# Kernel optimization log

Measured on AMD Instinct MI355X. Metric: run time of the kernel, lower is better.

The kernel has to match this reference:

```python
import jax, jax.numpy as jnp
import numpy as np
from jax import lax

H = 20  # hidden_size


def _rnn_layer(x_seq, h0, W_ih, W_hh, b_ih, b_hh):
    """Vanilla tanh RNN layer. x_seq: [B,T,D], h0: [B,H]. Returns ([B,T,H], [B,H])."""
    # Precompute input projection for all timesteps (the only large GEMM).
    xp = jnp.einsum('btd,hd->bth', x_seq, W_ih) + b_ih + b_hh  # [B,T,H]

    def step(h, xt):
        h = jnp.tanh(xt + h @ W_hh.T)
        return h, h

    h_last, hs = lax.scan(step, h0, jnp.swapaxes(xp, 0, 1))  # hs: [T,B,H]
    return jnp.swapaxes(hs, 0, 1), h_last


def setup_inputs() -> dict:
    key = jax.random.key(0)
    ks = jax.random.split(key, 12)
    B, T = 4096, 512
    s = 1.0 / np.sqrt(H)  # PyTorch default uniform(-1/sqrt(H), 1/sqrt(H))
    u = lambda k, shape: jax.random.uniform(k, shape, jnp.float32, -s, s)
    return {
        'x': jax.random.normal(ks[0], (B, T, 1), jnp.float32),
        'hidden': jax.random.normal(ks[1], (2, B, H), jnp.float32),
        'W_ih0': u(ks[2], (H, 1)),
        'W_hh0': u(ks[3], (H, H)),
        'b_ih0': u(ks[4], (H,)),
        'b_hh0': u(ks[5], (H,)),
        'W_ih1': u(ks[6], (H, H)),
        'W_hh1': u(ks[7], (H, H)),
        'b_ih1': u(ks[8], (H,)),
        'b_hh1': u(ks[9], (H,)),
        'fc_w': u(ks[10], (1, H)),
        'fc_b': u(ks[11], (1,)),
    }


def reference(x, hidden, W_ih0, W_hh0, b_ih0, b_hh0, W_ih1, W_hh1, b_ih1, b_hh1, fc_w, fc_b):
    # 2-layer vanilla RNN (eval mode: inter-layer dropout disabled)
    h0_seq, h0_last = _rnn_layer(x, hidden[0], W_ih0, W_hh0, b_ih0, b_hh0)
    h1_seq, h1_last = _rnn_layer(h0_seq, hidden[1], W_ih1, W_hh1, b_ih1, b_hh1)
    out = h1_seq[:, -1, :] @ fc_w.T + fc_b  # [B,1]
    new_hidden = jnp.stack([h0_last, h1_last], axis=0)  # [2,B,H]
    return out, new_hidden
```

## Files before the change

### kernel.cpp

```cpp
#include <hip/hip_runtime.h>


#define Bsz 4096
#define Tn  512
#define Hn  20
#define GB  3
#define XPAD 520
#define NTHREADS 64

typedef float v2 __attribute__((ext_vector_type(2)));

__device__ __forceinline__ float tanh_fast(float v) {
    float e = __expf(2.0f * v);
    return 1.0f - 2.0f * __builtin_amdgcn_rcpf(e + 1.0f);
}

#define DOT20P(acc, accb, W, H) do { \
    acc  = __builtin_elementwise_fma(W##0, H##0, acc);  \
    accb = __builtin_elementwise_fma(W##1, H##1, accb); \
    acc  = __builtin_elementwise_fma(W##2, H##2, acc);  \
    accb = __builtin_elementwise_fma(W##3, H##3, accb); \
    acc  = __builtin_elementwise_fma(W##4, H##4, acc);  \
    accb = __builtin_elementwise_fma(W##5, H##5, accb); \
    acc  = __builtin_elementwise_fma(W##6, H##6, acc);  \
    accb = __builtin_elementwise_fma(W##7, H##7, accb); \
    acc  = __builtin_elementwise_fma(W##8, H##8, acc);  \
    accb = __builtin_elementwise_fma(W##9, H##9, accb); \
} while (0)

#define LOAD_ROWP(W, ptr) \
    v2 W##0, W##1, W##2, W##3, W##4, W##5, W##6, W##7, W##8, W##9; \
    { const float4* _p = (const float4*)(ptr); \
      float4 _t; \
      _t = _p[0]; W##0 = (v2){_t.x, _t.y}; W##1 = (v2){_t.z, _t.w}; \
      _t = _p[1]; W##2 = (v2){_t.x, _t.y}; W##3 = (v2){_t.z, _t.w}; \
      _t = _p[2]; W##4 = (v2){_t.x, _t.y}; W##5 = (v2){_t.z, _t.w}; \
      _t = _p[3]; W##6 = (v2){_t.x, _t.y}; W##7 = (v2){_t.z, _t.w}; \
      _t = _p[4]; W##8 = (v2){_t.x, _t.y}; W##9 = (v2){_t.z, _t.w}; }

#define READ_H(H, base) \
    v2 H##0, H##1, H##2, H##3, H##4, H##5, H##6, H##7, H##8, H##9; \
    { const float4 _a = *(const float4*)((base) + 0);  \
      const float4 _b = *(const float4*)((base) + 4);  \
      const float4 _c = *(const float4*)((base) + 8);  \
      const float4 _d = *(const float4*)((base) + 12); \
      const float4 _e = *(const float4*)((base) + 16); \
      H##0 = (v2){_a.x, _a.y}; H##1 = (v2){_a.z, _a.w}; \
      H##2 = (v2){_b.x, _b.y}; H##3 = (v2){_b.z, _b.w}; \
      H##4 = (v2){_c.x, _c.y}; H##5 = (v2){_c.z, _c.w}; \
      H##6 = (v2){_d.x, _d.y}; H##7 = (v2){_d.z, _d.w}; \
      H##8 = (v2){_e.x, _e.y}; H##9 = (v2){_e.z, _e.w}; }

__global__ __launch_bounds__(NTHREADS)
__attribute__((amdgpu_waves_per_eu(1, 2)))
void rnn2_fused(const float* __restrict__ x,
                const float* __restrict__ hidden,
                const float* __restrict__ W_ih0,
                const float* __restrict__ W_hh0,
                const float* __restrict__ b_ih0,
                const float* __restrict__ b_hh0,
                const float* __restrict__ W_ih1,
                const float* __restrict__ W_hh1,
                const float* __restrict__ b_ih1,
                const float* __restrict__ b_hh1,
                const float* __restrict__ fc_w,
                const float* __restrict__ fc_b,
                float* __restrict__ out)
{
    const int tid = threadIdx.x;
    int g = tid / Hn;
    int j = tid - g * Hn;
    const bool lane_ok = (tid < GB * Hn);
    if (!lane_ok) g = GB - 1;
    const int  b        = blockIdx.x * GB + g;
    const bool b_ok     = (b < Bsz);
    const int  bl       = b_ok ? b : (Bsz - 1);
    const bool store_ok = lane_ok && b_ok;

    __shared__ float xs[GB][XPAD];
    __shared__ float hs[2][GB][Hn];

    LOAD_ROWP(w0, W_hh0 + j * Hn)
    LOAD_ROWP(w1, W_ih1 + j * Hn)
    LOAD_ROWP(w2, W_hh1 + j * Hn)

    const float wih0  = W_ih0[j];
    const float bias0 = b_ih0[j] + b_hh0[j];
    const float bias1 = b_ih1[j] + b_hh1[j];

    {
        const int bB = blockIdx.x * GB;
        #pragma unroll
        for (int r = 0; r < (GB * Tn) / (NTHREADS * 4); ++r) {
            const int c  = (r * NTHREADS + tid) * 4;
            const int gg = c >> 9;
            const int t  = c & (Tn - 1);
            const int bb = (bB + gg < Bsz) ? (bB + gg) : (Bsz - 1);
            float4 v = *(const float4*)(x + (long)bb * Tn + t);
            *(float4*)&xs[gg][t] = v;
        }
    }

    hs[0][g][j] = hidden[bl * Hn + j];
    hs[1][g][j] = hidden[(long)Bsz * Hn + bl * Hn + j];

    {
        READ_H(hA, &hs[0][g][0])
        v2 a0  = (v2){fmaf(xs[g][0], wih0, bias0), 0.f};
        v2 a0b = (v2){0.f, 0.f};
        DOT20P(a0, a0b, w0, hA);
        v2 s0 = a0 + a0b;
        hs[0][g][j] = tanh_fast(s0.x + s0.y);
    }

    #pragma unroll 1
    for (int i = 1; i < Tn; ++i) {
        READ_H(hA, &hs[0][g][0])
        READ_H(hB, &hs[1][g][0])

        const float xt = xs[g][i];

        v2 a0  = (v2){fmaf(xt, wih0, bias0), 0.f};
        v2 a0b = (v2){0.f, 0.f};
        v2 a1  = (v2){bias1, 0.f};
        v2 a1b = (v2){0.f, 0.f};
        v2 a2  = (v2){0.f, 0.f};
        v2 a2b = (v2){0.f, 0.f};
        DOT20P(a0, a0b, w0, hA);
        DOT20P(a1, a1b, w1, hA);
        DOT20P(a2, a2b, w2, hB);

        const v2 s0 = a0 + a0b;
        const v2 s1 = (a1 + a1b) + (a2 + a2b);
        const float n0 = tanh_fast(s0.x + s0.y);
        const float n1 = tanh_fast(s1.x + s1.y);
        hs[0][g][j] = n0;
        hs[1][g][j] = n1;
    }

    {
        READ_H(hA, &hs[0][g][0])
        READ_H(hB, &hs[1][g][0])
        v2 a1  = (v2){bias1, 0.f};
        v2 a1b = (v2){0.f, 0.f};
        v2 a2  = (v2){0.f, 0.f};
        v2 a2b = (v2){0.f, 0.f};
        DOT20P(a1, a1b, w1, hA);
        DOT20P(a2, a2b, w2, hB);
        const v2 s1 = (a1 + a1b) + (a2 + a2b);
        hs[1][g][j] = tanh_fast(s1.x + s1.y);
    }

    if (store_ok) {
        out[Bsz + (long)b * Hn + j]                  = hs[0][g][j];
        out[Bsz + (long)Bsz * Hn + (long)b * Hn + j] = hs[1][g][j];
        if (j == 0) {
            LOAD_ROWP(fw, fc_w)
            READ_H(hv, &hs[1][g][0])
            v2 aA = (v2){fc_b[0], 0.f};
            v2 aB = (v2){0.f, 0.f};
            DOT20P(aA, aB, fw, hv);
            const v2 s = aA + aB;
            out[b] = s.x + s.y;
        }
    }
}

extern "C" void kernel_launch(void* const* d_in, const int* in_sizes, int n_in,
                              void* d_out, int out_size, void* d_ws, size_t ws_size,
                              hipStream_t stream) {
    const float* x      = (const float*)d_in[0];
    const float* hidden = (const float*)d_in[1];
    const float* W_ih0  = (const float*)d_in[2];
    const float* W_hh0  = (const float*)d_in[3];
    const float* b_ih0  = (const float*)d_in[4];
    const float* b_hh0  = (const float*)d_in[5];
    const float* W_ih1  = (const float*)d_in[6];
    const float* W_hh1  = (const float*)d_in[7];
    const float* b_ih1  = (const float*)d_in[8];
    const float* b_hh1  = (const float*)d_in[9];
    const float* fc_w   = (const float*)d_in[10];
    const float* fc_b   = (const float*)d_in[11];

    const int nblocks = (Bsz + GB - 1) / GB;
    rnn2_fused<<<nblocks, NTHREADS, 0, stream>>>(
        x, hidden, W_ih0, W_hh0, b_ih0, b_hh0,
        W_ih1, W_hh1, b_ih1, b_hh1, fc_w, fc_b, (float*)d_out);
}
```

Baseline: 141.6 us.

## Software-pipeline LDS hidden-state exchange with inline asm and partial waitcnts

Replaces the compiler-generated LDS writes and reads of the hidden states with inline-asm ds_write/ds_read sequences. Each layer's new state is written and the next step's state and input are prefetched right after that layer's tanh. Partial lgkmcnt waits let the layer-1 dot product overlap with the layer-0 reads, aiming to hide LDS latency on the serial recurrence path. It relies on in-wave LDS ordering without barriers, and hand-written waitcnt counts make it fragile. Idle lanes get distinct j values to avoid write conflicts.

```diff
diff --git a/kernel.cpp b/kernel.cpp
--- a/kernel.cpp
+++ b/kernel.cpp
@@ -1,4 +1,5 @@
 #include <hip/hip_runtime.h>
+#include <stdint.h>
 
 
 #define Bsz 4096
@@ -15,17 +16,17 @@
     return 1.0f - 2.0f * __builtin_amdgcn_rcpf(e + 1.0f);
 }
 
-#define DOT20P(acc, accb, W, H) do { \
-    acc  = __builtin_elementwise_fma(W##0, H##0, acc);  \
-    accb = __builtin_elementwise_fma(W##1, H##1, accb); \
-    acc  = __builtin_elementwise_fma(W##2, H##2, acc);  \
-    accb = __builtin_elementwise_fma(W##3, H##3, accb); \
-    acc  = __builtin_elementwise_fma(W##4, H##4, acc);  \
-    accb = __builtin_elementwise_fma(W##5, H##5, accb); \
-    acc  = __builtin_elementwise_fma(W##6, H##6, acc);  \
-    accb = __builtin_elementwise_fma(W##7, H##7, accb); \
-    acc  = __builtin_elementwise_fma(W##8, H##8, acc);  \
-    accb = __builtin_elementwise_fma(W##9, H##9, accb); \
+#define DOT20Q(acc, accb, W, C0, C1, C2, C3, C4) do { \
+    acc  = __builtin_elementwise_fma(W##0, (v2){(C0).x,(C0).y}, acc);  \
+    accb = __builtin_elementwise_fma(W##1, (v2){(C0).z,(C0).w}, accb); \
+    acc  = __builtin_elementwise_fma(W##2, (v2){(C1).x,(C1).y}, acc);  \
+    accb = __builtin_elementwise_fma(W##3, (v2){(C1).z,(C1).w}, accb); \
+    acc  = __builtin_elementwise_fma(W##4, (v2){(C2).x,(C2).y}, acc);  \
+    accb = __builtin_elementwise_fma(W##5, (v2){(C2).z,(C2).w}, accb); \
+    acc  = __builtin_elementwise_fma(W##6, (v2){(C3).x,(C3).y}, acc);  \
+    accb = __builtin_elementwise_fma(W##7, (v2){(C3).z,(C3).w}, accb); \
+    acc  = __builtin_elementwise_fma(W##8, (v2){(C4).x,(C4).y}, acc);  \
+    accb = __builtin_elementwise_fma(W##9, (v2){(C4).z,(C4).w}, accb); \
 } while (0)
 
 #define LOAD_ROWP(W, ptr) \
@@ -37,19 +38,6 @@
       _t = _p[2]; W##4 = (v2){_t.x, _t.y}; W##5 = (v2){_t.z, _t.w}; \
       _t = _p[3]; W##6 = (v2){_t.x, _t.y}; W##7 = (v2){_t.z, _t.w}; \
       _t = _p[4]; W##8 = (v2){_t.x, _t.y}; W##9 = (v2){_t.z, _t.w}; }
-
-#define READ_H(H, base) \
-    v2 H##0, H##1, H##2, H##3, H##4, H##5, H##6, H##7, H##8, H##9; \
-    { const float4 _a = *(const float4*)((base) + 0);  \
-      const float4 _b = *(const float4*)((base) + 4);  \
-      const float4 _c = *(const float4*)((base) + 8);  \
-      const float4 _d = *(const float4*)((base) + 12); \
-      const float4 _e = *(const float4*)((base) + 16); \
-      H##0 = (v2){_a.x, _a.y}; H##1 = (v2){_a.z, _a.w}; \
-      H##2 = (v2){_b.x, _b.y}; H##3 = (v2){_b.z, _b.w}; \
-      H##4 = (v2){_c.x, _c.y}; H##5 = (v2){_c.z, _c.w}; \
-      H##6 = (v2){_d.x, _d.y}; H##7 = (v2){_d.z, _d.w}; \
-      H##8 = (v2){_e.x, _e.y}; H##9 = (v2){_e.z, _e.w}; }
 
 __global__ __launch_bounds__(NTHREADS)
 __attribute__((amdgpu_waves_per_eu(1, 2)))
@@ -71,19 +59,18 @@
     int g = tid / Hn;
     int j = tid - g * Hn;
     const bool lane_ok = (tid < GB * Hn);
-    if (!lane_ok) g = GB - 1;
+    if (!lane_ok) { g = GB - 1; j = tid - 60; }
     const int  b        = blockIdx.x * GB + g;
     const bool b_ok     = (b < Bsz);
     const int  bl       = b_ok ? b : (Bsz - 1);
     const bool store_ok = lane_ok && b_ok;
 
-    __shared__ float xs[GB][XPAD];
-    __shared__ float hs[2][GB][Hn];
+    __shared__ __align__(16) float xs[GB][XPAD];
+    __shared__ __align__(16) float hs[2][GB][Hn];
 
     LOAD_ROWP(w0, W_hh0 + j * Hn)
     LOAD_ROWP(w1, W_ih1 + j * Hn)
     LOAD_ROWP(w2, W_hh1 + j * Hn)
-
     const float wih0  = W_ih0[j];
     const float bias0 = b_ih0[j] + b_hh0[j];
     const float bias1 = b_ih1[j] + b_hh1[j];
@@ -101,69 +88,145 @@
         }
     }
 
+    const float h1i = hidden[(long)Bsz * Hn + bl * Hn + j];
     hs[0][g][j] = hidden[bl * Hn + j];
-    hs[1][g][j] = hidden[(long)Bsz * Hn + bl * Hn + j];
-
+    hs[1][g][j] = h1i;
+
+    uint32_t h0_base = (uint32_t)(uintptr_t)&hs[0][g][0];
+    uint32_t h0_mine = (uint32_t)(uintptr_t)&hs[0][g][j];
+    uint32_t h1_base = (uint32_t)(uintptr_t)&hs[1][g][0];
+    uint32_t h1_mine = (uint32_t)(uintptr_t)&hs[1][g][j];
+    uint32_t x_addr  = (uint32_t)(uintptr_t)&xs[g][2];
+
+    float n0_keep;
     {
-        READ_H(hA, &hs[0][g][0])
+        const float4 p0 = *(const float4*)&hs[0][g][0];
+        const float4 p1 = *(const float4*)&hs[0][g][4];
+        const float4 p2 = *(const float4*)&hs[0][g][8];
+        const float4 p3 = *(const float4*)&hs[0][g][12];
+        const float4 p4 = *(const float4*)&hs[0][g][16];
         v2 a0  = (v2){fmaf(xs[g][0], wih0, bias0), 0.f};
         v2 a0b = (v2){0.f, 0.f};
-        DOT20P(a0, a0b, w0, hA);
-        v2 s0 = a0 + a0b;
-        hs[0][g][j] = tanh_fast(s0.x + s0.y);
-    }
-
+        DOT20Q(a0, a0b, w0, p0, p1, p2, p3, p4);
+        const v2 s0 = a0 + a0b;
+        n0_keep = tanh_fast(s0.x + s0.y);
+    }
+
+    asm volatile("s_waitcnt lgkmcnt(0)" ::: "memory");
+    __builtin_amdgcn_sched_barrier(0);
+
+    float4 c0, c1, c2, c3, c4;
+    float4 d0, d1, d2, d3, d4;
+    float  xt;
+
+    asm volatile(
+        "ds_write_b32 %7, %8\n\t"
+        "ds_read_b128 %0, %6 offset:0\n\t"
+        "ds_read_b128 %1, %6 offset:16\n\t"
+        "ds_read_b128 %2, %6 offset:32\n\t"
+        "ds_read_b128 %3, %6 offset:48\n\t"
+        "ds_read_b128 %4, %6 offset:64\n\t"
+        "ds_read_b32  %5, %9\n\t"
+        : "=&v"(c0), "=&v"(c1), "=&v"(c2), "=&v"(c3), "=&v"(c4), "=&v"(xt)
+        : "v"(h0_base), "v"(h0_mine), "v"(n0_keep),
+          "v"((uint32_t)(uintptr_t)&xs[g][1])
+        : "memory");
+    asm volatile(
+        "ds_read_b128 %0, %5 offset:0\n\t"
+        "ds_read_b128 %1, %5 offset:16\n\t"
+        "ds_read_b128 %2, %5 offset:32\n\t"
+        "ds_read_b128 %3, %5 offset:48\n\t"
+        "ds_read_b128 %4, %5 offset:64\n\t"
+        : "=&v"(d0), "=&v"(d1), "=&v"(d2), "=&v"(d3), "=&v"(d4)
+        : "v"(h1_base)
+        : "memory");
+    asm volatile("s_waitcnt lgkmcnt(5)" ::: "memory");
+    __builtin_amdgcn_sched_barrier(0);
+
+    float n1_keep = 0.f;
     #pragma unroll 1
     for (int i = 1; i < Tn; ++i) {
-        READ_H(hA, &hs[0][g][0])
-        READ_H(hB, &hs[1][g][0])
-
-        const float xt = xs[g][i];
-
         v2 a0  = (v2){fmaf(xt, wih0, bias0), 0.f};
         v2 a0b = (v2){0.f, 0.f};
         v2 a1  = (v2){bias1, 0.f};
         v2 a1b = (v2){0.f, 0.f};
+        DOT20Q(a0, a0b, w0, c0, c1, c2, c3, c4);
+        DOT20Q(a1, a1b, w1, c0, c1, c2, c3, c4);
+        const v2 s0 = a0 + a0b;
+        const float n0 = tanh_fast(s0.x + s0.y);
+        n0_keep = n0;
+
+        asm volatile(
+            "ds_write_b32 %7, %8\n\t"
+            "ds_read_b128 %0, %6 offset:0\n\t"
+            "ds_read_b128 %1, %6 offset:16\n\t"
+            "ds_read_b128 %2, %6 offset:32\n\t"
+            "ds_read_b128 %3, %6 offset:48\n\t"
+            "ds_read_b128 %4, %6 offset:64\n\t"
+            "ds_read_b32  %5, %9\n\t"
+            : "=&v"(c0), "=&v"(c1), "=&v"(c2), "=&v"(c3), "=&v"(c4), "=&v"(xt)
+            : "v"(h0_base), "v"(h0_mine), "v"(n0), "v"(x_addr)
+            : "memory");
+        x_addr += 4;
+
+        asm volatile("s_waitcnt lgkmcnt(7)" ::: "memory");
+        __builtin_amdgcn_sched_barrier(0);
+
         v2 a2  = (v2){0.f, 0.f};
         v2 a2b = (v2){0.f, 0.f};
-        DOT20P(a0, a0b, w0, hA);
-        DOT20P(a1, a1b, w1, hA);
-        DOT20P(a2, a2b, w2, hB);
-
-        const v2 s0 = a0 + a0b;
+        DOT20Q(a2, a2b, w2, d0, d1, d2, d3, d4);
         const v2 s1 = (a1 + a1b) + (a2 + a2b);
-        const float n0 = tanh_fast(s0.x + s0.y);
         const float n1 = tanh_fast(s1.x + s1.y);
-        hs[0][g][j] = n0;
-        hs[1][g][j] = n1;
-    }
-
+        n1_keep = n1;
+
+        asm volatile(
+            "ds_write_b32 %5, %6\n\t"
+            "ds_read_b128 %0, %7 offset:0\n\t"
+            "ds_read_b128 %1, %7 offset:16\n\t"
+            "ds_read_b128 %2, %7 offset:32\n\t"
+            "ds_read_b128 %3, %7 offset:48\n\t"
+            "ds_read_b128 %4, %7 offset:64\n\t"
+            : "=&v"(d0), "=&v"(d1), "=&v"(d2), "=&v"(d3), "=&v"(d4)
+            : "v"(h1_mine), "v"(n1), "v"(h1_base)
+            : "memory");
+
+        asm volatile("s_waitcnt lgkmcnt(6)" ::: "memory");
+        __builtin_amdgcn_sched_barrier(0);
+    }
+
+    asm volatile("s_waitcnt lgkmcnt(0)" ::: "memory");
+    __builtin_amdgcn_sched_barrier(0);
+    float n1_last;
     {
-        READ_H(hA, &hs[0][g][0])
-        READ_H(hB, &hs[1][g][0])
         v2 a1  = (v2){bias1, 0.f};
         v2 a1b = (v2){0.f, 0.f};
         v2 a2  = (v2){0.f, 0.f};
         v2 a2b = (v2){0.f, 0.f};
-        DOT20P(a1, a1b, w1, hA);
-        DOT20P(a2, a2b, w2, hB);
+        DOT20Q(a1, a1b, w1, c0, c1, c2, c3, c4);
+        DOT20Q(a2, a2b, w2, d0, d1, d2, d3, d4);
         const v2 s1 = (a1 + a1b) + (a2 + a2b);
-        hs[1][g][j] = tanh_fast(s1.x + s1.y);
-    }
+        n1_last = tanh_fast(s1.x + s1.y);
+    }
+    hs[1][g][j] = n1_last;
 
     if (store_ok) {
-        out[Bsz + (long)b * Hn + j]                  = hs[0][g][j];
-        out[Bsz + (long)Bsz * Hn + (long)b * Hn + j] = hs[1][g][j];
+        out[Bsz + (long)b * Hn + j]                  = n0_keep;
+        out[Bsz + (long)Bsz * Hn + (long)b * Hn + j] = n1_last;
         if (j == 0) {
             LOAD_ROWP(fw, fc_w)
-            READ_H(hv, &hs[1][g][0])
+            const float4 v0 = *(const float4*)&hs[1][g][0];
+            const float4 v1 = *(const float4*)&hs[1][g][4];
+            const float4 v2q = *(const float4*)&hs[1][g][8];
+            const float4 v3 = *(const float4*)&hs[1][g][12];
+            const float4 v4 = *(const float4*)&hs[1][g][16];
             v2 aA = (v2){fc_b[0], 0.f};
             v2 aB = (v2){0.f, 0.f};
-            DOT20P(aA, aB, fw, hv);
+            DOT20Q(aA, aB, fw, v0, v1, v2q, v3, v4);
             const v2 s = aA + aB;
             out[b] = s.x + s.y;
         }
     }
+    (void)n1_keep;
 }
 
 extern "C" void kernel_launch(void* const* d_in, const int* in_sizes, int n_in,
```

Result: slower. 211.8 us (+49.5%).

## Interleave two independent batch groups per wave with software-prefetched hidden state

Applied to the files above, without the earlier changes.

Each 64-thread block now processes six batch rows as two interleaved groups of three, alternating their recurrent steps so one group's dot products overlap the other's LDS writes and reads. Hidden-state vectors and the next input are reloaded right after each store, so they are ready before the next use. Final states are taken from registers instead of shared memory. This halves the block count and lengthens each wave's serial chain, trading parallelism for instruction-level overlap.

```diff
diff --git a/kernel.cpp b/kernel.cpp
--- a/kernel.cpp
+++ b/kernel.cpp
@@ -4,7 +4,7 @@
 #define Bsz 4096
 #define Tn  512
 #define Hn  20
-#define GB  3
+#define GPW 6
 #define XPAD 520
 #define NTHREADS 64
 
@@ -38,18 +38,20 @@
       _t = _p[3]; W##6 = (v2){_t.x, _t.y}; W##7 = (v2){_t.z, _t.w}; \
       _t = _p[4]; W##8 = (v2){_t.x, _t.y}; W##9 = (v2){_t.z, _t.w}; }
 
-#define READ_H(H, base) \
-    v2 H##0, H##1, H##2, H##3, H##4, H##5, H##6, H##7, H##8, H##9; \
-    { const float4 _a = *(const float4*)((base) + 0);  \
-      const float4 _b = *(const float4*)((base) + 4);  \
-      const float4 _c = *(const float4*)((base) + 8);  \
-      const float4 _d = *(const float4*)((base) + 12); \
-      const float4 _e = *(const float4*)((base) + 16); \
-      H##0 = (v2){_a.x, _a.y}; H##1 = (v2){_a.z, _a.w}; \
-      H##2 = (v2){_b.x, _b.y}; H##3 = (v2){_b.z, _b.w}; \
-      H##4 = (v2){_c.x, _c.y}; H##5 = (v2){_c.z, _c.w}; \
-      H##6 = (v2){_d.x, _d.y}; H##7 = (v2){_d.z, _d.w}; \
-      H##8 = (v2){_e.x, _e.y}; H##9 = (v2){_e.z, _e.w}; }
+#define DECL_H(H) v2 H##0, H##1, H##2, H##3, H##4, H##5, H##6, H##7, H##8, H##9;
+
+#define READ_INTO(H, base) do { \
+    const float4 _a = *(const float4*)((base) + 0);  \
+    const float4 _b = *(const float4*)((base) + 4);  \
+    const float4 _c = *(const float4*)((base) + 8);  \
+    const float4 _d = *(const float4*)((base) + 12); \
+    const float4 _e = *(const float4*)((base) + 16); \
+    H##0 = (v2){_a.x, _a.y}; H##1 = (v2){_a.z, _a.w}; \
+    H##2 = (v2){_b.x, _b.y}; H##3 = (v2){_b.z, _b.w}; \
+    H##4 = (v2){_c.x, _c.y}; H##5 = (v2){_c.z, _c.w}; \
+    H##6 = (v2){_d.x, _d.y}; H##7 = (v2){_d.z, _d.w}; \
+    H##8 = (v2){_e.x, _e.y}; H##9 = (v2){_e.z, _e.w}; \
+} while (0)
 
 __global__ __launch_bounds__(NTHREADS)
 __attribute__((amdgpu_waves_per_eu(1, 2)))
@@ -70,98 +72,167 @@
     const int tid = threadIdx.x;
     int g = tid / Hn;
     int j = tid - g * Hn;
-    const bool lane_ok = (tid < GB * Hn);
-    if (!lane_ok) g = GB - 1;
-    const int  b        = blockIdx.x * GB + g;
-    const bool b_ok     = (b < Bsz);
-    const int  bl       = b_ok ? b : (Bsz - 1);
-    const bool store_ok = lane_ok && b_ok;
-
-    __shared__ float xs[GB][XPAD];
-    __shared__ float hs[2][GB][Hn];
+    const bool lane_ok = (tid < 3 * Hn);
+    if (!lane_ok) { g = 2; j = tid - 60; }
+
+    const int  bA   = blockIdx.x * GPW + g;
+    const int  bB   = bA + 3;
+    const bool okA  = lane_ok && (bA < Bsz);
+    const bool okB  = lane_ok && (bB < Bsz);
+    const int  blA  = (bA < Bsz) ? bA : (Bsz - 1);
+    const int  blB  = (bB < Bsz) ? bB : (Bsz - 1);
+
+    __shared__ float xs[GPW][XPAD];
+    __shared__ float hs[2][GPW][Hn];
 
     LOAD_ROWP(w0, W_hh0 + j * Hn)
     LOAD_ROWP(w1, W_ih1 + j * Hn)
     LOAD_ROWP(w2, W_hh1 + j * Hn)
-
     const float wih0  = W_ih0[j];
     const float bias0 = b_ih0[j] + b_hh0[j];
     const float bias1 = b_ih1[j] + b_hh1[j];
 
     {
-        const int bB = blockIdx.x * GB;
+        const int bBase = blockIdx.x * GPW;
         #pragma unroll
-        for (int r = 0; r < (GB * Tn) / (NTHREADS * 4); ++r) {
+        for (int r = 0; r < (GPW * Tn) / (NTHREADS * 4); ++r) {
             const int c  = (r * NTHREADS + tid) * 4;
             const int gg = c >> 9;
             const int t  = c & (Tn - 1);
-            const int bb = (bB + gg < Bsz) ? (bB + gg) : (Bsz - 1);
+            const int bb = (bBase + gg < Bsz) ? (bBase + gg) : (Bsz - 1);
             float4 v = *(const float4*)(x + (long)bb * Tn + t);
             *(float4*)&xs[gg][t] = v;
         }
     }
 
-    hs[0][g][j] = hidden[bl * Hn + j];
-    hs[1][g][j] = hidden[(long)Bsz * Hn + bl * Hn + j];
-
-    {
-        READ_H(hA, &hs[0][g][0])
-        v2 a0  = (v2){fmaf(xs[g][0], wih0, bias0), 0.f};
-        v2 a0b = (v2){0.f, 0.f};
-        DOT20P(a0, a0b, w0, hA);
-        v2 s0 = a0 + a0b;
-        hs[0][g][j] = tanh_fast(s0.x + s0.y);
-    }
-
+    hs[0][g][j]     = hidden[blA * Hn + j];
+    hs[1][g][j]     = hidden[(long)Bsz * Hn + blA * Hn + j];
+    hs[0][g + 3][j] = hidden[blB * Hn + j];
+    hs[1][g + 3][j] = hidden[(long)Bsz * Hn + blB * Hn + j];
+
+    DECL_H(hA0) DECL_H(hA1) DECL_H(hB0) DECL_H(hB1)
+    READ_INTO(hA0, &hs[0][g][0]);
+    READ_INTO(hA1, &hs[1][g][0]);
+    READ_INTO(hB0, &hs[0][g + 3][0]);
+    READ_INTO(hB1, &hs[1][g + 3][0]);
+
+    {
+        v2 a  = (v2){fmaf(xs[g][0], wih0, bias0), 0.f};
+        v2 ab = (v2){0.f, 0.f};
+        DOT20P(a, ab, w0, hA0);
+        const v2 s = a + ab;
+        hs[0][g][j] = tanh_fast(s.x + s.y);
+        READ_INTO(hA0, &hs[0][g][0]);
+        v2 c  = (v2){fmaf(xs[g + 3][0], wih0, bias0), 0.f};
+        v2 cb = (v2){0.f, 0.f};
+        DOT20P(c, cb, w0, hB0);
+        const v2 t = c + cb;
+        hs[0][g + 3][j] = tanh_fast(t.x + t.y);
+        READ_INTO(hB0, &hs[0][g + 3][0]);
+    }
+    float xtA = xs[g][1];
+    float xtB = xs[g + 3][1];
+
+    float n0A = 0.f, n0B = 0.f;
     #pragma unroll 1
     for (int i = 1; i < Tn; ++i) {
-        READ_H(hA, &hs[0][g][0])
-        READ_H(hB, &hs[1][g][0])
-
-        const float xt = xs[g][i];
-
-        v2 a0  = (v2){fmaf(xt, wih0, bias0), 0.f};
-        v2 a0b = (v2){0.f, 0.f};
+        const int tn2 = (i + 1 < Tn) ? (i + 1) : (Tn - 1);
+
+        {
+            v2 a0  = (v2){fmaf(xtA, wih0, bias0), 0.f};
+            v2 a0b = (v2){0.f, 0.f};
+            v2 a1  = (v2){bias1, 0.f};
+            v2 a1b = (v2){0.f, 0.f};
+            v2 a2  = (v2){0.f, 0.f};
+            v2 a2b = (v2){0.f, 0.f};
+            DOT20P(a0, a0b, w0, hA0);
+            DOT20P(a1, a1b, w1, hA0);
+            DOT20P(a2, a2b, w2, hA1);
+            const v2 s0 = a0 + a0b;
+            const v2 s1 = (a1 + a1b) + (a2 + a2b);
+            const float n0 = tanh_fast(s0.x + s0.y);
+            const float n1 = tanh_fast(s1.x + s1.y);
+            n0A = n0;
+            hs[0][g][j] = n0;
+            hs[1][g][j] = n1;
+            READ_INTO(hA0, &hs[0][g][0]);
+            READ_INTO(hA1, &hs[1][g][0]);
+            xtA = xs[g][tn2];
+        }
+        {
+            v2 a0  = (v2){fmaf(xtB, wih0, bias0), 0.f};
+            v2 a0b = (v2){0.f, 0.f};
+            v2 a1  = (v2){bias1, 0.f};
+            v2 a1b = (v2){0.f, 0.f};
+            v2 a2  = (v2){0.f, 0.f};
+            v2 a2b = (v2){0.f, 0.f};
+            DOT20P(a0, a0b, w0, hB0);
+            DOT20P(a1, a1b, w1, hB0);
+            DOT20P(a2, a2b, w2, hB1);
+            const v2 s0 = a0 + a0b;
+            const v2 s1 = (a1 + a1b) + (a2 + a2b);
+            const float n0 = tanh_fast(s0.x + s0.y);
+            const float n1 = tanh_fast(s1.x + s1.y);
+            n0B = n0;
+            hs[0][g + 3][j] = n0;
+            hs[1][g + 3][j] = n1;
+            READ_INTO(hB0, &hs[0][g + 3][0]);
+            READ_INTO(hB1, &hs[1][g + 3][0]);
+            xtB = xs[g + 3][tn2];
+        }
+    }
+
+    float n1A, n1B;
+    {
         v2 a1  = (v2){bias1, 0.f};
         v2 a1b = (v2){0.f, 0.f};
         v2 a2  = (v2){0.f, 0.f};
         v2 a2b = (v2){0.f, 0.f};
-        DOT20P(a0, a0b, w0, hA);
-        DOT20P(a1, a1b, w1, hA);
-        DOT20P(a2, a2b, w2, hB);
-
-        const v2 s0 = a0 + a0b;
-        const v2 s1 = (a1 + a1b) + (a2 + a2b);
-        const float n0 = tanh_fast(s0.x + s0.y);
-        const float n1 = tanh_fast(s1.x + s1.y);
-        hs[0][g][j] = n0;
-        hs[1][g][j] = n1;
-    }
-
-    {
-        READ_H(hA, &hs[0][g][0])
-        READ_H(hB, &hs[1][g][0])
+        DOT20P(a1, a1b, w1, hA0);
+        DOT20P(a2, a2b, w2, hA1);
+        const v2 s = (a1 + a1b) + (a2 + a2b);
+        n1A = tanh_fast(s.x + s.y);
+        hs[1][g][j] = n1A;
+    }
+    {
         v2 a1  = (v2){bias1, 0.f};
         v2 a1b = (v2){0.f, 0.f};
         v2 a2  = (v2){0.f, 0.f};
         v2 a2b = (v2){0.f, 0.f};
-        DOT20P(a1, a1b, w1, hA);
-        DOT20P(a2, a2b, w2, hB);
-        const v2 s1 = (a1 + a1b) + (a2 + a2b);
-        hs[1][g][j] = tanh_fast(s1.x + s1.y);
-    }
-
-    if (store_ok) {
-        out[Bsz + (long)b * Hn + j]                  = hs[0][g][j];
-        out[Bsz + (long)Bsz * Hn + (long)b * Hn + j] = hs[1][g][j];
-        if (j == 0) {
-            LOAD_ROWP(fw, fc_w)
-            READ_H(hv, &hs[1][g][0])
+        DOT20P(a1, a1b, w1, hB0);
+        DOT20P(a2, a2b, w2, hB1);
+        const v2 s = (a1 + a1b) + (a2 + a2b);
+        n1B = tanh_fast(s.x + s.y);
+        hs[1][g + 3][j] = n1B;
+    }
+
+    if (okA) {
+        out[Bsz + (long)bA * Hn + j]                  = n0A;
+        out[Bsz + (long)Bsz * Hn + (long)bA * Hn + j] = n1A;
+    }
+    if (okB) {
+        out[Bsz + (long)bB * Hn + j]                  = n0B;
+        out[Bsz + (long)Bsz * Hn + (long)bB * Hn + j] = n1B;
+    }
+    if (j == 0) {
+        LOAD_ROWP(fw, fc_w)
+        if (okA) {
+            DECL_H(hv)
+            READ_INTO(hv, &hs[1][g][0]);
             v2 aA = (v2){fc_b[0], 0.f};
             v2 aB = (v2){0.f, 0.f};
             DOT20P(aA, aB, fw, hv);
             const v2 s = aA + aB;
-            out[b] = s.x + s.y;
+            out[bA] = s.x + s.y;
+        }
+        if (okB) {
+            DECL_H(hv)
+            READ_INTO(hv, &hs[1][g + 3][0]);
+            v2 aA = (v2){fc_b[0], 0.f};
+            v2 aB = (v2){0.f, 0.f};
+            DOT20P(aA, aB, fw, hv);
+            const v2 s = aA + aB;
+            out[bB] = s.x + s.y;
         }
     }
 }
@@ -182,7 +253,7 @@
     const float* fc_w   = (const float*)d_in[10];
     const float* fc_b   = (const float*)d_in[11];
 
-    const int nblocks = (Bsz + GB - 1) / GB;
+    const int nblocks = (Bsz + GPW - 1) / GPW;
     rnn2_fused<<<nblocks, NTHREADS, 0, stream>>>(
         x, hidden, W_ih0, W_hh0, b_ih0, b_hh0,
         W_ih1, W_hh1, b_ih1, b_hh1, fc_w, fc_b, (float*)d_out);
```

After: 163.8 us. +15.7%, slower.
